# Kernel tuning notes

Hardware: AMD Instinct MI355X
Metric: run time of the kernel (lower is better)

The kernel has to match this reference:

```python
import jax, jax.numpy as jnp
import numpy as np

IN_F, H1, H2, NC = 784, 1024, 1024, 10
BATCH = 32
EPS = 0.1


def setup_inputs() -> dict:
    key = jax.random.key(0)
    ks = jax.random.split(key, 8)
    x = jax.random.normal(ks[0], (BATCH, IN_F), jnp.float32)
    y = jax.random.randint(ks[1], (BATCH,), 0, NC)
    W1 = jax.random.normal(ks[2], (H1, IN_F), jnp.float32) / np.float32(np.sqrt(IN_F))
    b1 = jax.random.normal(ks[3], (H1,), jnp.float32) * 0.01
    W2 = jax.random.normal(ks[4], (H2, H1), jnp.float32) / np.float32(np.sqrt(H1))
    b2 = jax.random.normal(ks[5], (H2,), jnp.float32) * 0.01
    W3 = jax.random.normal(ks[6], (NC, H2), jnp.float32) / np.float32(np.sqrt(H2))
    b3 = jax.random.normal(ks[7], (NC,), jnp.float32) * 0.01
    return dict(x=x, y=y, W1=W1, b1=b1, W2=W2, b2=b2, W3=W3, b3=b3)


def _relu_coeffs(zl, zu):
    # d = 1 where zl>=0, zu/(zu-zl) where crossing, 0 where zu<=0 (as in select_layer)
    I = (zl < 0) & (zu > 0)
    d = jnp.where(zl >= 0, 1.0, jnp.where(I, zu / (zu - zl), 0.0))
    lI = jnp.where(I, zl, 0.0)  # zl restricted to crossing set I
    return d, lI


def reference(x, y, W1, b1, W2, b2, W3, b3):
    eps = jnp.float32(EPS)
    # ---- layer-1 preactivation bounds (InfBall fval) ----
    nom1 = x @ W1.T + b1                              # [B,H1]
    r1 = eps * jnp.abs(W1).sum(1)                     # [H1]
    zl1, zu1 = nom1 - r1, nom1 + r1
    d1, l1m = _relu_coeffs(zl1, zu1)                  # [B,H1]

    # ---- layer-2 preactivation bounds via dual (transpose) propagation, nu = I ----
    nu1 = W2[None, :, :] * d1[:, None, :]             # [B,H2,H1]  (D1 W2^T rows)
    V0 = jnp.einsum('bji,ik->bjk', nu1, W1)           # [B,H2,IN]
    A = jnp.einsum('bjk,bk->bj', V0, x) + b2 + nu1 @ b1
    E = eps * jnp.abs(V0).sum(-1)
    crossl = jnp.einsum('bji,bi->bj', jax.nn.relu(-nu1), l1m)
    crossu = jnp.einsum('bji,bi->bj', jax.nn.relu(nu1), l1m)
    zl2 = A - E + crossl
    zu2 = A + E - crossu
    d2, l2m = _relu_coeffs(zl2, zu2)                  # [B,H2]

    # ---- final robust bounds: c[b,j,:] = e_{y_b} - e_j ----
    eye = jnp.eye(NC, dtype=x.dtype)
    c = eye[y][:, None, :] - eye[None, :, :]          # [B,NC,NC]
    nu2 = (c @ W3) * d2[:, None, :]                   # [B,NC,H2]
    nu1f = (nu2 @ W2) * d1[:, None, :]                # [B,NC,H1]
    V0f = nu1f @ W1                                   # [B,NC,IN]
    Af = jnp.einsum('bjk,bk->bj', V0f, x) + c @ b3 + nu2 @ b2 + nu1f @ b1
    Ef = eps * jnp.abs(V0f).sum(-1)
    crossf = (jnp.einsum('bji,bi->bj', jax.nn.relu(-nu2), l2m)
              + jnp.einsum('bji,bi->bj', jax.nn.relu(-nu1f), l1m))
    J = Af - Ef + crossf                              # lower bound of c^T z
    return -J                                         # f: upper bound of z_j - z_y, [B,NC]
```

## Files before the change

kernel.cpp:

```cpp
#include <hip/hip_runtime.h>
#include <math.h>

#define B    32
#define INF  784
#define H1   1024
#define H2   1024
#define NC   10
#define EPSV 0.1f

typedef __attribute__((ext_vector_type(8))) short short8;
typedef __attribute__((ext_vector_type(4))) float floatx4;

__device__ inline ushort bf16_rne(float f) {
  uint u = __builtin_bit_cast(uint, f);
  u += 0x7FFFu + ((u >> 16) & 1u);
  return (ushort)(u >> 16);
}
__device__ inline uint pack2(float a, float b) {
  return (uint)bf16_rne(a) | ((uint)bf16_rne(b) << 16);
}
__device__ inline uint scale_pack(uint u, float d0, float d1v) {
  float f0 = __builtin_bit_cast(float, u << 16) * d0;
  float f1 = __builtin_bit_cast(float, u & 0xFFFF0000u) * d1v;
  uint r0 = __builtin_bit_cast(uint, f0) + 0x8000u;
  uint r1 = __builtin_bit_cast(uint, f1) + 0x8000u;
  return __builtin_amdgcn_perm(r1, r0, 0x07060302u);
}

__global__ __launch_bounds__(256) void k_pre(
    const float* __restrict__ x, const float* __restrict__ W1,
    const float* __restrict__ b1, const float* __restrict__ W2,
    ushort* __restrict__ W1F, ushort* __restrict__ W2F,
    float* __restrict__ d1B, float* __restrict__ t1B, float* __restrict__ dnB,
    float* __restrict__ Ezero)
{
  __shared__ float red[4][B + 1];
  __shared__ float Ts[4][32][17];
  int bid = blockIdx.x;
  int t = threadIdx.x;
  if (bid < 64) {
    int jt = bid;
    int lane = t & 63, c0 = t >> 6;
    int l15 = lane & 15, quad = lane >> 4;
    for (int c = c0; c < 32; c += 4) {
      const float* src = &W2[(size_t)(jt * 16 + l15) * H1 + c * 32 + quad * 8];
      float4 v0 = *reinterpret_cast<const float4*>(src);
      float4 v1 = *reinterpret_cast<const float4*>(src + 4);
      uint4 o;
      o.x = pack2(v0.x, v0.y); o.y = pack2(v0.z, v0.w);
      o.z = pack2(v1.x, v1.y); o.w = pack2(v1.z, v1.w);
      *reinterpret_cast<uint4*>(&W2F[((size_t)(c * 64 + jt) * 64 + lane) * 8]) = o;
    }
  } else if (bid < 114) {
    int mt = bid - 64;
    int w = t >> 6, lane = t & 63;
    int l15 = lane & 15, quad = lane >> 4;
    if (mt >= 49) {
      uint4 z; z.x = 0; z.y = 0; z.z = 0; z.w = 0;
      for (int cg = 0; cg < 8; cg++) {
        int c = cg * 4 + w;
        *reinterpret_cast<uint4*>(&W1F[((size_t)(c * 50 + mt) * 64 + lane) * 8]) = z;
      }
    } else {
      int col0 = mt * 16;
      for (int cg = 0; cg < 8; cg++) {
        int c = cg * 4 + w;
#pragma unroll
        for (int p = 0; p < 8; p++) {
          int r = p * 4 + (lane >> 4);
          Ts[w][r][lane & 15] = W1[(size_t)(c * 32 + r) * INF + col0 + (lane & 15)];
        }
        float f[8];
#pragma unroll
        for (int e = 0; e < 8; e++) f[e] = Ts[w][quad * 8 + e][l15];
        uint4 o;
        o.x = pack2(f[0], f[1]); o.y = pack2(f[2], f[3]);
        o.z = pack2(f[4], f[5]); o.w = pack2(f[6], f[7]);
        *reinterpret_cast<uint4*>(&W1F[((size_t)(c * 50 + mt) * 64 + lane) * 8]) = o;
      }
    }
  } else if (bid < 1138) {
    int i = bid - 114;
    const float* w = W1 + (size_t)i * INF;
    float acc[B];
#pragma unroll
    for (int b = 0; b < B; b++) acc[b] = 0.f;
    float wabs = 0.f;
    for (int k = t; k < INF; k += 256) {
      float wv = w[k];
      wabs += fabsf(wv);
#pragma unroll
      for (int b = 0; b < B; b++) acc[b] = fmaf(x[b * INF + k], wv, acc[b]);
    }
#pragma unroll
    for (int off = 32; off > 0; off >>= 1) {
#pragma unroll
      for (int b = 0; b < B; b++) acc[b] += __shfl_down(acc[b], off, 64);
      wabs += __shfl_down(wabs, off, 64);
    }
    int wave = t >> 6, lane = t & 63;
    if (lane == 0) {
#pragma unroll
      for (int b = 0; b < B; b++) red[wave][b] = acc[b];
      red[wave][B] = wabs;
    }
    __syncthreads();
    if (t < B) {
      float s = red[0][t] + red[1][t] + red[2][t] + red[3][t];
      float r = EPSV * (red[0][B] + red[1][B] + red[2][B] + red[3][B]);
      float nom = s + b1[i];
      float zl = nom - r, zu = nom + r;
      float d, l;
      if (zl >= 0.f)      { d = 1.f;            l = 0.f; }
      else if (zu > 0.f)  { d = zu / (zu - zl); l = zl;  }
      else                { d = 0.f;            l = 0.f; }
      d1B[(size_t)t * H1 + i] = d;
      t1B[(size_t)t * H1 + i] = d * l;
      dnB[(size_t)t * H1 + i] = d * nom;
    }
  } else {
    int zb = bid - 1138;
    for (int idx = t; idx < 8192; idx += 256) {
      int pos = zb * 8192 + idx;
      if (pos < 54272) Ezero[pos] = 0.f;
    }
  }
}

#define K3_LOAD(c, A, Bv) do {                                                  \
  _Pragma("unroll")                                                             \
  for (int ni = 0; ni < 2; ni++)                                                \
    Bv[ni] = *reinterpret_cast<const uint4*>(bBase + (size_t)(c) * 32768 + ni * 512); \
  _Pragma("unroll")                                                             \
  for (int mi = 0; mi < 5; mi++)                                                \
    A[mi] = *reinterpret_cast<const uint4*>(aBase + (size_t)(c) * 25600 + mi * 512); \
} while (0)

#define K3F_COMP(c, A, Bv, DsRow, accB) do {                                    \
  float4 dv0 = *reinterpret_cast<const float4*>(&DsRow[(c) * 32]);              \
  float4 dv1 = *reinterpret_cast<const float4*>(&DsRow[(c) * 32 + 4]);          \
  short8 bfr[2];                                                                \
  _Pragma("unroll")                                                             \
  for (int ni = 0; ni < 2; ni++) {                                              \
    uint4 sb;                                                                   \
    sb.x = scale_pack(Bv[ni].x, dv0.x, dv0.y);                                  \
    sb.y = scale_pack(Bv[ni].y, dv0.z, dv0.w);                                  \
    sb.z = scale_pack(Bv[ni].z, dv1.x, dv1.y);                                  \
    sb.w = scale_pack(Bv[ni].w, dv1.z, dv1.w);                                  \
    bfr[ni] = __builtin_bit_cast(short8, sb);                                   \
  }                                                                             \
  _Pragma("unroll")                                                             \
  for (int mi = 0; mi < 5; mi++) {                                              \
    short8 af = __builtin_bit_cast(short8, A[mi]);                              \
    _Pragma("unroll")                                                           \
    for (int ni = 0; ni < 2; ni++)                                              \
      accB[mi][ni] = __builtin_amdgcn_mfma_f32_16x16x32_bf16(af, bfr[ni], accB[mi][ni], 0, 0, 0); \
  }                                                                             \
} while (0)

__global__ __launch_bounds__(256, 3) void k3(
    const ushort* __restrict__ W1F, const ushort* __restrict__ W2F,
    const float* __restrict__ d1B, float* __restrict__ E)
{
  int b0 = blockIdx.z * 2;
  int t = threadIdx.x, w = t >> 6, lane = t & 63;
  int quad = lane >> 4, l15 = lane & 15;
  int mt0 = blockIdx.x * 5;
  int jt0 = blockIdx.y * 8 + w * 2;

  __shared__ float Ds[2][H1];
  for (int idx = t; idx < 2 * H1; idx += 256)
    Ds[idx >> 10][idx & 1023] = d1B[(size_t)(b0 + (idx >> 10)) * H1 + (idx & 1023)];
  __syncthreads();

  const ushort* aBase = W1F + ((size_t)mt0 * 64 + lane) * 8;
  const ushort* bBase = W2F + ((size_t)jt0 * 64 + lane) * 8;
  const float* Ds0 = &Ds[0][quad * 8];
  const float* Ds1 = &Ds[1][quad * 8];

  floatx4 acc[2][5][2];
#pragma unroll
  for (int bb = 0; bb < 2; bb++)
#pragma unroll
    for (int mi = 0; mi < 5; mi++)
#pragma unroll
      for (int ni = 0; ni < 2; ni++) acc[bb][mi][ni] = (floatx4){0.f, 0.f, 0.f, 0.f};

  uint4 a0[5], b0v[2], a1[5], b1v[2];
  K3_LOAD(0, a0, b0v);
  K3_LOAD(1, a1, b1v);
  for (int c = 0; c < 30; c += 2) {
    K3F_COMP(c, a0, b0v, Ds0, acc[0]);
    K3F_COMP(c, a0, b0v, Ds1, acc[1]);
    K3_LOAD(c + 2, a0, b0v);
    K3F_COMP(c + 1, a1, b1v, Ds0, acc[0]);
    K3F_COMP(c + 1, a1, b1v, Ds1, acc[1]);
    if (c + 3 < 32) K3_LOAD(c + 3, a1, b1v);
  }
  K3F_COMP(30, a0, b0v, Ds0, acc[0]);
  K3F_COMP(30, a0, b0v, Ds1, acc[1]);
  K3F_COMP(31, a1, b1v, Ds0, acc[0]);
  K3F_COMP(31, a1, b1v, Ds1, acc[1]);

#pragma unroll
  for (int bb = 0; bb < 2; bb++) {
#pragma unroll
    for (int ni = 0; ni < 2; ni++) {
      float s = 0.f;
#pragma unroll
      for (int mi = 0; mi < 5; mi++)
#pragma unroll
        for (int r = 0; r < 4; r++) s += fabsf(acc[bb][mi][ni][r]);
      s += __shfl_xor(s, 16, 64);
      s += __shfl_xor(s, 32, 64);
      if (lane < 16) {
        int j = (jt0 + ni) * 16 + l15;
        atomicAdd(&E[(size_t)j * B + b0 + bb], EPSV * s);
      }
    }
  }
}

__global__ __launch_bounds__(256) void k245a(
    const float* __restrict__ W2, const float* __restrict__ b2,
    const float* __restrict__ dnB, const float* __restrict__ t1B,
    const float* __restrict__ E, const float* __restrict__ W3,
    const int* __restrict__ y,
    float* __restrict__ nu2T, float* __restrict__ F2)
{
  int j = blockIdx.x;
  int t = threadIdx.x;
  int wave = t >> 6, lane = t & 63;
  int b0 = wave * 8;
  float aA[8] = {}, aCl[8] = {}, aCu[8] = {};
  const float* __restrict__ w2 = W2 + (size_t)j * H1;
  for (int i = lane; i < H1; i += 64) {
    float wv = w2[i];
    float wp = fmaxf(wv, 0.f), wn = fmaxf(-wv, 0.f);
#pragma unroll
    for (int r = 0; r < 8; r++) {
      float dv = dnB[(size_t)(b0 + r) * H1 + i];
      float tv = t1B[(size_t)(b0 + r) * H1 + i];
      aA[r]  = fmaf(wv, dv, aA[r]);
      aCl[r] = fmaf(wn, tv, aCl[r]);
      aCu[r] = fmaf(wp, tv, aCu[r]);
    }
  }
#pragma unroll
  for (int off = 32; off > 0; off >>= 1) {
#pragma unroll
    for (int r = 0; r < 8; r++) {
      aA[r]  += __shfl_down(aA[r],  off, 64);
      aCl[r] += __shfl_down(aCl[r], off, 64);
      aCu[r] += __shfl_down(aCu[r], off, 64);
    }
  }
  __shared__ float sA[B], sCl[B], sCu[B];
  __shared__ float sd2[B], st2[B], sdb[B], swy[B], sw3[NC];
  float bj = b2[j];
  if (lane == 0) {
#pragma unroll
    for (int r = 0; r < 8; r++) {
      sA [b0 + r] = aA[r] + bj;
      sCl[b0 + r] = aCl[r];
      sCu[b0 + r] = aCu[r];
    }
  }
  if (t >= 64 && t < 96)   swy[t - 64]  = W3[(size_t)y[t - 64] * H2 + j];
  if (t >= 128 && t < 138) sw3[t - 128] = W3[(size_t)(t - 128) * H2 + j];
  __syncthreads();
  if (t < B) {
    float a = sA[t], e = E[(size_t)j * B + t];
    float zl = a - e + sCl[t];
    float zu = a + e - sCu[t];
    float d, l;
    if (zl >= 0.f)      { d = 1.f;            l = 0.f; }
    else if (zu > 0.f)  { d = zu / (zu - zl); l = zl;  }
    else                { d = 0.f;            l = 0.f; }
    sd2[t] = d;
    st2[t] = d * l;
    sdb[t] = d * bj;
  }
  __syncthreads();
  for (int tt = t; tt < B * NC; tt += 256) {
    int b = tt / NC, jc = tt - b * NC;
    float cw = swy[b] - sw3[jc];
    float d2v = sd2[b];
    nu2T[((size_t)b * H2 + j) * 12 + jc] = cw * d2v;
    float val = cw * sdb[b] + fmaxf(-cw, 0.f) * st2[b];
    atomicAdd(&F2[((size_t)(j & 63) * B + b) * NC + jc], val);
  }
}

__global__ __launch_bounds__(256) void k5b1(
    const float* __restrict__ W2, const float* __restrict__ nu2T,
    float* __restrict__ hpart)
{
  int t = threadIdx.x;
  int i1 = blockIdx.x * 512 + t * 2;
  int b = blockIdx.y, s = blockIdx.z;
  const float* __restrict__ nrowb = nu2T + ((size_t)b * H2 + s * 128) * 12;
  const float* __restrict__ w2b = W2 + (size_t)s * 128 * H1 + i1;
  float h0[NC] = {}, h1[NC] = {};
  for (int i2 = 0; i2 < 128; i2++) {
    float2 wv = *reinterpret_cast<const float2*>(&w2b[(size_t)i2 * H1]);
    const float* __restrict__ nrow = nrowb + i2 * 12;
#pragma unroll
    for (int j = 0; j < NC; j++) {
      h0[j] = fmaf(nrow[j], wv.x, h0[j]);
      h1[j] = fmaf(nrow[j], wv.y, h1[j]);
    }
  }
#pragma unroll
  for (int j = 0; j < NC; j++) {
    float2 o; o.x = h0[j]; o.y = h1[j];
    *reinterpret_cast<float2*>(&hpart[(((size_t)s * B + b) * NC + j) * H1 + i1]) = o;
  }
}

__global__ __launch_bounds__(256) void k5b2(
    const float* __restrict__ hpart,
    const float* __restrict__ d1B, const float* __restrict__ t1B,
    const float* __restrict__ dnB,
    float* __restrict__ nu1fT, float* __restrict__ F)
{
  int t = threadIdx.x;
  int i1 = blockIdx.x * 256 + t;
  int b = blockIdx.y;
  float d1v = d1B[(size_t)b * H1 + i1];
  float t1v = t1B[(size_t)b * H1 + i1];
  float dnv = dnB[(size_t)b * H1 + i1];
  float sn[NC], c1[NC];
#pragma unroll
  for (int j = 0; j < NC; j++) {
    float hv = 0.f;
#pragma unroll
    for (int s = 0; s < 8; s++)
      hv += hpart[(((size_t)s * B + b) * NC + j) * H1 + i1];
    nu1fT[((size_t)b * H1 + i1) * 12 + j] = hv * d1v;
    sn[j] = hv * dnv;
    c1[j] = fmaxf(-hv, 0.f) * t1v;
  }
#pragma unroll
  for (int off = 32; off > 0; off >>= 1) {
#pragma unroll
    for (int j = 0; j < NC; j++) {
      sn[j] += __shfl_down(sn[j], off, 64);
      c1[j] += __shfl_down(c1[j], off, 64);
    }
  }
  __shared__ float red[4][2 * NC];
  int wave = t >> 6, lane = t & 63;
  if (lane == 0) {
#pragma unroll
    for (int j = 0; j < NC; j++) { red[wave][j] = sn[j]; red[wave][NC + j] = c1[j]; }
  }
  __syncthreads();
  if (t < NC) {
    float s = 0.f;
    for (int w = 0; w < 4; w++) s += red[w][t] + red[w][NC + t];
    atomicAdd(&F[b * NC + t], s);
  }
}

__global__ __launch_bounds__(128) void k5c1(
    const float* __restrict__ W1, const float* __restrict__ nu1fT,
    float* __restrict__ ppart)
{
  int t = threadIdx.x;
  bool valid = (t < 112);
  int k = blockIdx.x * 112 + (valid ? t : 0);
  int b = blockIdx.y, s = blockIdx.z;
  const float* __restrict__ nrowb = nu1fT + ((size_t)b * H1 + s * 128) * 12;
  const float* __restrict__ w1b = W1 + (size_t)s * 128 * INF + k;
  float acc[NC] = {};
  for (int i1 = 0; i1 < 128; i1++) {
    float w1v = w1b[(size_t)i1 * INF];
    const float* __restrict__ nrow = nrowb + i1 * 12;
#pragma unroll
    for (int j = 0; j < NC; j++) acc[j] = fmaf(nrow[j], w1v, acc[j]);
  }
  if (valid) {
#pragma unroll
    for (int j = 0; j < NC; j++)
      ppart[(((size_t)s * B + b) * NC + j) * INF + k] = acc[j];
  }
}

__global__ __launch_bounds__(256) void k5c2_out(
    const float* __restrict__ ppart, const float* __restrict__ F,
    const float* __restrict__ F2, const float* __restrict__ b3,
    const int* __restrict__ y, float* __restrict__ out)
{
  int b = blockIdx.x;
  int t = threadIdx.x;
  float e[NC] = {};
  for (int k = t; k < INF; k += 256) {
#pragma unroll
    for (int j = 0; j < NC; j++) {
      float v = 0.f;
#pragma unroll
      for (int s = 0; s < 8; s++)
        v += ppart[(((size_t)s * B + b) * NC + j) * INF + k];
      e[j] += fabsf(v);
    }
  }
#pragma unroll
  for (int off = 32; off > 0; off >>= 1) {
#pragma unroll
    for (int j = 0; j < NC; j++) e[j] += __shfl_down(e[j], off, 64);
  }
  __shared__ float red[4][NC];
  int wave = t >> 6, lane = t & 63;
  if (lane == 0) {
#pragma unroll
    for (int j = 0; j < NC; j++) red[wave][j] = e[j];
  }
  __syncthreads();
  if (t < NC) {
    float ef = 0.f;
    for (int w = 0; w < 4; w++) ef += red[w][t];
    float s = F[b * NC + t];
    for (int slot = 0; slot < 64; slot++)
      s += F2[((size_t)slot * B + b) * NC + t];
    int yb = y[b];
    s += b3[yb] - b3[t];
    out[b * NC + t] = EPSV * ef - s;
  }
}

extern "C" void kernel_launch(void* const* d_in, const int* in_sizes, int n_in,
                              void* d_out, int out_size, void* d_ws, size_t ws_size,
                              hipStream_t stream) {
  const float* x  = (const float*)d_in[0];
  const int*   y  = (const int*)  d_in[1];
  const float* W1 = (const float*)d_in[2];
  const float* b1 = (const float*)d_in[3];
  const float* W2 = (const float*)d_in[4];
  const float* b2 = (const float*)d_in[5];
  const float* W3 = (const float*)d_in[6];
  const float* b3 = (const float*)d_in[7];
  float* out = (float*)d_out;
  float* ws  = (float*)d_ws;

  float* d1B  = ws;
  float* t1B  = ws + 32768;
  float* dnB  = ws + 65536;
  float* E    = ws + 196608;
  float* F    = ws + 229376;
  float* F2   = ws + 230400;
  float* nu2T = ws + 328704;
  ushort* W2F = (ushort*)(ws + 721920);
  ushort* W1F = (ushort*)(ws + 1246208);
  float* nu1fT = ws + 328704;
  float* hpart = ws + 721920;
  float* ppart = ws + 721920;

  k_pre<<<1145, 256, 0, stream>>>(x, W1, b1, W2, W1F, W2F, d1B, t1B, dnB, E);
  k3<<<dim3(10, 8, 16), 256, 0, stream>>>(W1F, W2F, d1B, E);
  k245a<<<H2, 256, 0, stream>>>(W2, b2, dnB, t1B, E, W3, y, nu2T, F2);
  k5b1<<<dim3(2, B, 8), 256, 0, stream>>>(W2, nu2T, hpart);
  k5b2<<<dim3(4, B), 256, 0, stream>>>(hpart, d1B, t1B, dnB, nu1fT, F);
  k5c1<<<dim3(7, B, 8), 128, 0, stream>>>(W1, nu1fT, ppart);
  k5c2_out<<<B, 256, 0, stream>>>(ppart, F, F2, b3, y, out);
}
```

Baseline: 214.4 us.

## Register-block two rows/batches per thread and parallelize final reduction with last-block finish

k245a now processes two output rows per block, so each dnB/t1B load is reused for two W2 rows. k5b1 and k5c1 each handle two batch elements per thread, so every W2/W1 load is reused twice and the grid is halved. The final reduction kernel is split across 7x32 blocks that atomically accumulate into EfB, and a global counter lets the last block compute the outputs. The zeroing range is extended to cover EfB and the counter; the trade is more register pressure and fewer blocks in exchange for less redundant memory traffic.

New measurement: 242.1 us. 1.13x slower.

```diff
diff --git a/kernel.cpp b/kernel.cpp
--- a/kernel.cpp
+++ b/kernel.cpp
@@ -27,7 +27,7 @@
   return __builtin_amdgcn_perm(r1, r0, 0x07060302u);
 }
 
-__global__ __launch_bounds__(256) void k_pre(
+__global__ __launch_bounds__(256) void k_pre50(
     const float* __restrict__ x, const float* __restrict__ W1,
     const float* __restrict__ b1, const float* __restrict__ W2,
     ushort* __restrict__ W1F, ushort* __restrict__ W2F,
@@ -122,7 +122,7 @@
     int zb = bid - 1138;
     for (int idx = t; idx < 8192; idx += 256) {
       int pos = zb * 8192 + idx;
-      if (pos < 54272) Ezero[pos] = 0.f;
+      if (pos < 55552) Ezero[pos] = 0.f;
     }
   }
 }
@@ -228,66 +228,85 @@
     const int* __restrict__ y,
     float* __restrict__ nu2T, float* __restrict__ F2)
 {
-  int j = blockIdx.x;
+  int j0 = blockIdx.x * 2;
   int t = threadIdx.x;
   int wave = t >> 6, lane = t & 63;
   int b0 = wave * 8;
-  float aA[8] = {}, aCl[8] = {}, aCu[8] = {};
-  const float* __restrict__ w2 = W2 + (size_t)j * H1;
+  float aA[2][8] = {}, aCl[2][8] = {}, aCu[2][8] = {};
+  const float* __restrict__ w2r0 = W2 + (size_t)j0 * H1;
+  const float* __restrict__ w2r1 = W2 + (size_t)(j0 + 1) * H1;
   for (int i = lane; i < H1; i += 64) {
-    float wv = w2[i];
-    float wp = fmaxf(wv, 0.f), wn = fmaxf(-wv, 0.f);
+    float wv0 = w2r0[i], wv1 = w2r1[i];
+    float wp0 = fmaxf(wv0, 0.f), wn0 = fmaxf(-wv0, 0.f);
+    float wp1 = fmaxf(wv1, 0.f), wn1 = fmaxf(-wv1, 0.f);
 #pragma unroll
     for (int r = 0; r < 8; r++) {
       float dv = dnB[(size_t)(b0 + r) * H1 + i];
       float tv = t1B[(size_t)(b0 + r) * H1 + i];
-      aA[r]  = fmaf(wv, dv, aA[r]);
-      aCl[r] = fmaf(wn, tv, aCl[r]);
-      aCu[r] = fmaf(wp, tv, aCu[r]);
-    }
-  }
-#pragma unroll
-  for (int off = 32; off > 0; off >>= 1) {
-#pragma unroll
-    for (int r = 0; r < 8; r++) {
-      aA[r]  += __shfl_down(aA[r],  off, 64);
-      aCl[r] += __shfl_down(aCl[r], off, 64);
-      aCu[r] += __shfl_down(aCu[r], off, 64);
-    }
-  }
-  __shared__ float sA[B], sCl[B], sCu[B];
-  __shared__ float sd2[B], st2[B], sdb[B], swy[B], sw3[NC];
-  float bj = b2[j];
+      aA [0][r] = fmaf(wv0, dv, aA [0][r]);
+      aCl[0][r] = fmaf(wn0, tv, aCl[0][r]);
+      aCu[0][r] = fmaf(wp0, tv, aCu[0][r]);
+      aA [1][r] = fmaf(wv1, dv, aA [1][r]);
+      aCl[1][r] = fmaf(wn1, tv, aCl[1][r]);
+      aCu[1][r] = fmaf(wp1, tv, aCu[1][r]);
+    }
+  }
+#pragma unroll
+  for (int off = 32; off > 0; off >>= 1)
+#pragma unroll
+    for (int jj = 0; jj < 2; jj++)
+#pragma unroll
+      for (int r = 0; r < 8; r++) {
+        aA [jj][r] += __shfl_down(aA [jj][r], off, 64);
+        aCl[jj][r] += __shfl_down(aCl[jj][r], off, 64);
+        aCu[jj][r] += __shfl_down(aCu[jj][r], off, 64);
+      }
+  __shared__ float sA[2][B], sCl[2][B], sCu[2][B];
+  __shared__ float sd2[2][B], st2[2][B], sdb[2][B], swy[2][B], sw3[2][NC];
   if (lane == 0) {
 #pragma unroll
-    for (int r = 0; r < 8; r++) {
-      sA [b0 + r] = aA[r] + bj;
-      sCl[b0 + r] = aCl[r];
-      sCu[b0 + r] = aCu[r];
-    }
-  }
-  if (t >= 64 && t < 96)   swy[t - 64]  = W3[(size_t)y[t - 64] * H2 + j];
-  if (t >= 128 && t < 138) sw3[t - 128] = W3[(size_t)(t - 128) * H2 + j];
+    for (int jj = 0; jj < 2; jj++) {
+      float bj = b2[j0 + jj];
+#pragma unroll
+      for (int r = 0; r < 8; r++) {
+        sA [jj][b0 + r] = aA [jj][r] + bj;
+        sCl[jj][b0 + r] = aCl[jj][r];
+        sCu[jj][b0 + r] = aCu[jj][r];
+      }
+    }
+  }
+  if (t >= 128 && t < 192) {
+    int jj = (t - 128) >> 5, b = (t - 128) & 31;
+    swy[jj][b] = W3[(size_t)y[b] * H2 + j0 + jj];
+  }
+  if (t >= 192 && t < 212) {
+    int jj = (t - 192) / NC, c = (t - 192) % NC;
+    sw3[jj][c] = W3[(size_t)c * H2 + j0 + jj];
+  }
   __syncthreads();
-  if (t < B) {
-    float a = sA[t], e = E[(size_t)j * B + t];
-    float zl = a - e + sCl[t];
-    float zu = a + e - sCu[t];
+  if (t < 2 * B) {
+    int jj = t >> 5, b = t & 31;
+    float bj = b2[j0 + jj];
+    float a = sA[jj][b], e = E[(size_t)(j0 + jj) * B + b];
+    float zl = a - e + sCl[jj][b];
+    float zu = a + e - sCu[jj][b];
     float d, l;
     if (zl >= 0.f)      { d = 1.f;            l = 0.f; }
     else if (zu > 0.f)  { d = zu / (zu - zl); l = zl;  }
     else                { d = 0.f;            l = 0.f; }
-    sd2[t] = d;
-    st2[t] = d * l;
-    sdb[t] = d * bj;
+    sd2[jj][b] = d;
+    st2[jj][b] = d * l;
+    sdb[jj][b] = d * bj;
   }
   __syncthreads();
-  for (int tt = t; tt < B * NC; tt += 256) {
-    int b = tt / NC, jc = tt - b * NC;
-    float cw = swy[b] - sw3[jc];
-    float d2v = sd2[b];
+  for (int tt = t; tt < 2 * B * NC; tt += 256) {
+    int jj = tt / (B * NC), rem = tt - jj * B * NC;
+    int b = rem / NC, jc = rem - b * NC;
+    int j = j0 + jj;
+    float cw = swy[jj][b] - sw3[jj][jc];
+    float d2v = sd2[jj][b];
     nu2T[((size_t)b * H2 + j) * 12 + jc] = cw * d2v;
-    float val = cw * sdb[b] + fmaxf(-cw, 0.f) * st2[b];
+    float val = cw * sdb[jj][b] + fmaxf(-cw, 0.f) * st2[jj][b];
     atomicAdd(&F2[((size_t)(j & 63) * B + b) * NC + jc], val);
   }
 }
@@ -298,24 +317,31 @@
 {
   int t = threadIdx.x;
   int i1 = blockIdx.x * 512 + t * 2;
-  int b = blockIdx.y, s = blockIdx.z;
-  const float* __restrict__ nrowb = nu2T + ((size_t)b * H2 + s * 128) * 12;
+  int bp = blockIdx.y * 2, s = blockIdx.z;
+  const float* __restrict__ n0b = nu2T + ((size_t)bp * H2 + s * 128) * 12;
+  const float* __restrict__ n1b = nu2T + ((size_t)(bp + 1) * H2 + s * 128) * 12;
   const float* __restrict__ w2b = W2 + (size_t)s * 128 * H1 + i1;
-  float h0[NC] = {}, h1[NC] = {};
+  float h[2][2][NC] = {};
   for (int i2 = 0; i2 < 128; i2++) {
     float2 wv = *reinterpret_cast<const float2*>(&w2b[(size_t)i2 * H1]);
-    const float* __restrict__ nrow = nrowb + i2 * 12;
+    const float* __restrict__ n0 = n0b + i2 * 12;
+    const float* __restrict__ n1 = n1b + i2 * 12;
 #pragma unroll
     for (int j = 0; j < NC; j++) {
-      h0[j] = fmaf(nrow[j], wv.x, h0[j]);
-      h1[j] = fmaf(nrow[j], wv.y, h1[j]);
-    }
-  }
-#pragma unroll
-  for (int j = 0; j < NC; j++) {
-    float2 o; o.x = h0[j]; o.y = h1[j];
-    *reinterpret_cast<float2*>(&hpart[(((size_t)s * B + b) * NC + j) * H1 + i1]) = o;
-  }
+      float a0 = n0[j], a1 = n1[j];
+      h[0][0][j] = fmaf(a0, wv.x, h[0][0][j]);
+      h[0][1][j] = fmaf(a0, wv.y, h[0][1][j]);
+      h[1][0][j] = fmaf(a1, wv.x, h[1][0][j]);
+      h[1][1][j] = fmaf(a1, wv.y, h[1][1][j]);
+    }
+  }
+#pragma unroll
+  for (int bb = 0; bb < 2; bb++)
+#pragma unroll
+    for (int j = 0; j < NC; j++) {
+      float2 o; o.x = h[bb][0][j]; o.y = h[bb][1][j];
+      *reinterpret_cast<float2*>(&hpart[(((size_t)s * B + bp + bb) * NC + j) * H1 + i1]) = o;
+    }
 }
 
 __global__ __launch_bounds__(256) void k5b2(
@@ -370,62 +396,77 @@
   int t = threadIdx.x;
   bool valid = (t < 112);
   int k = blockIdx.x * 112 + (valid ? t : 0);
-  int b = blockIdx.y, s = blockIdx.z;
-  const float* __restrict__ nrowb = nu1fT + ((size_t)b * H1 + s * 128) * 12;
+  int bp = blockIdx.y * 2, s = blockIdx.z;
+  const float* __restrict__ n0b = nu1fT + ((size_t)bp * H1 + s * 128) * 12;
+  const float* __restrict__ n1b = nu1fT + ((size_t)(bp + 1) * H1 + s * 128) * 12;
   const float* __restrict__ w1b = W1 + (size_t)s * 128 * INF + k;
-  float acc[NC] = {};
+  float acc[2][NC] = {};
   for (int i1 = 0; i1 < 128; i1++) {
     float w1v = w1b[(size_t)i1 * INF];
-    const float* __restrict__ nrow = nrowb + i1 * 12;
-#pragma unroll
-    for (int j = 0; j < NC; j++) acc[j] = fmaf(nrow[j], w1v, acc[j]);
+    const float* __restrict__ n0 = n0b + i1 * 12;
+    const float* __restrict__ n1 = n1b + i1 * 12;
+#pragma unroll
+    for (int j = 0; j < NC; j++) {
+      acc[0][j] = fmaf(n0[j], w1v, acc[0][j]);
+      acc[1][j] = fmaf(n1[j], w1v, acc[1][j]);
+    }
   }
   if (valid) {
 #pragma unroll
-    for (int j = 0; j < NC; j++)
-      ppart[(((size_t)s * B + b) * NC + j) * INF + k] = acc[j];
-  }
-}
-
-__global__ __launch_bounds__(256) void k5c2_out(
-    const float* __restrict__ ppart, const float* __restrict__ F,
-    const float* __restrict__ F2, const float* __restrict__ b3,
-    const int* __restrict__ y, float* __restrict__ out)
-{
-  int b = blockIdx.x;
+    for (int bb = 0; bb < 2; bb++)
+#pragma unroll
+      for (int j = 0; j < NC; j++)
+        ppart[(((size_t)s * B + bp + bb) * NC + j) * INF + k] = acc[bb][j];
+  }
+}
+
+__global__ __launch_bounds__(128) void k5c2p(
+    const float* __restrict__ ppart, float* __restrict__ EfB,
+    uint* __restrict__ cnt,
+    const float* __restrict__ F, const float* __restrict__ F2,
+    const float* __restrict__ b3, const int* __restrict__ y,
+    float* __restrict__ out)
+{
   int t = threadIdx.x;
-  float e[NC] = {};
-  for (int k = t; k < INF; k += 256) {
-#pragma unroll
-    for (int j = 0; j < NC; j++) {
-      float v = 0.f;
-#pragma unroll
-      for (int s = 0; s < 8; s++)
-        v += ppart[(((size_t)s * B + b) * NC + j) * INF + k];
-      e[j] += fabsf(v);
-    }
+  bool valid = (t < 112);
+  int k = blockIdx.x * 112 + (valid ? t : 0);
+  int b = blockIdx.y;
+  float e[NC];
+#pragma unroll
+  for (int j = 0; j < NC; j++) {
+    float v = 0.f;
+#pragma unroll
+    for (int s = 0; s < 8; s++)
+      v += ppart[(((size_t)s * B + b) * NC + j) * INF + k];
+    e[j] = valid ? fabsf(v) : 0.f;
   }
 #pragma unroll
   for (int off = 32; off > 0; off >>= 1) {
 #pragma unroll
     for (int j = 0; j < NC; j++) e[j] += __shfl_down(e[j], off, 64);
   }
-  __shared__ float red[4][NC];
+  __shared__ float red[2][NC];
   int wave = t >> 6, lane = t & 63;
   if (lane == 0) {
 #pragma unroll
     for (int j = 0; j < NC; j++) red[wave][j] = e[j];
   }
   __syncthreads();
-  if (t < NC) {
-    float ef = 0.f;
-    for (int w = 0; w < 4; w++) ef += red[w][t];
-    float s = F[b * NC + t];
-    for (int slot = 0; slot < 64; slot++)
-      s += F2[((size_t)slot * B + b) * NC + t];
-    int yb = y[b];
-    s += b3[yb] - b3[t];
-    out[b * NC + t] = EPSV * ef - s;
+  if (t < NC) atomicAdd(&EfB[b * NC + t], red[0][t] + red[1][t]);
+  __threadfence();
+  __shared__ uint done;
+  if (t == 0) done = atomicAdd(cnt, 1u);
+  __syncthreads();
+  if (done == 7 * B - 1) {
+    for (int tt = t; tt < B * NC; tt += 128) {
+      int bb = tt / NC, j = tt - bb * NC;
+      float s = F[tt];
+      for (int slot = 0; slot < 64; slot++)
+        s += F2[((size_t)slot * B + bb) * NC + j];
+      s += b3[y[bb]] - b3[j];
+      float ef = atomicAdd(&EfB[tt], 0.f);
+      out[tt] = EPSV * ef - s;
+    }
   }
 }
 
@@ -449,6 +490,8 @@
   float* E    = ws + 196608;
   float* F    = ws + 229376;
   float* F2   = ws + 230400;
+  float* EfB  = ws + 250880;
+  uint*  cnt  = (uint*)(ws + 251904);
   float* nu2T = ws + 328704;
   ushort* W2F = (ushort*)(ws + 721920);
   ushort* W1F = (ushort*)(ws + 1246208);
@@ -456,11 +499,11 @@
   float* hpart = ws + 721920;
   float* ppart = ws + 721920;
 
-  k_pre<<<1145, 256, 0, stream>>>(x, W1, b1, W2, W1F, W2F, d1B, t1B, dnB, E);
+  k_pre50<<<1145, 256, 0, stream>>>(x, W1, b1, W2, W1F, W2F, d1B, t1B, dnB, E);
   k3<<<dim3(10, 8, 16), 256, 0, stream>>>(W1F, W2F, d1B, E);
-  k245a<<<H2, 256, 0, stream>>>(W2, b2, dnB, t1B, E, W3, y, nu2T, F2);
-  k5b1<<<dim3(2, B, 8), 256, 0, stream>>>(W2, nu2T, hpart);
+  k245a<<<512, 256, 0, stream>>>(W2, b2, dnB, t1B, E, W3, y, nu2T, F2);
+  k5b1<<<dim3(2, 16, 8), 256, 0, stream>>>(W2, nu2T, hpart);
   k5b2<<<dim3(4, B), 256, 0, stream>>>(hpart, d1B, t1B, dnB, nu1fT, F);
-  k5c1<<<dim3(7, B, 8), 128, 0, stream>>>(W1, nu1fT, ppart);
-  k5c2_out<<<B, 256, 0, stream>>>(ppart, F, F2, b3, y, out);
-}
+  k5c1<<<dim3(7, 16, 8), 128, 0, stream>>>(W1, nu1fT, ppart);
+  k5c2p<<<dim3(7, B), 128, 0, stream>>>(ppart, EfB, cnt, F, F2, b3, y, out);
+}
```
